# Performance work log

Measured on AMD Instinct MI355X. Metric: run time of the kernel, lower is better.

Reference implementation:

```python
import jax, jax.numpy as jnp
import numpy as np

D = 1024      # d_model
H = 16        # num_heads
HW = D // H   # head_width = 64
FF = 4 * D    # hidden_dim = 4096
BATCH = 2
T = 2048
EPS = 1e-5


def layer_norm(x, g, b):
    mu = jnp.mean(x, axis=-1, keepdims=True)
    var = jnp.mean(jnp.square(x - mu), axis=-1, keepdims=True)
    return (x - mu) * jax.lax.rsqrt(var + EPS) * g + b


def setup_inputs() -> dict:
    key = jax.random.key(0)
    ks = jax.random.split(key, 7)
    s = 0.02
    return {
        "x": jax.random.normal(ks[0], (BATCH, T, D), dtype=jnp.float32),
        "Wq": jax.random.normal(ks[1], (D, D), dtype=jnp.float32) * s,
        "Wk": jax.random.normal(ks[2], (D, D), dtype=jnp.float32) * s,
        "Wv": jax.random.normal(ks[3], (D, D), dtype=jnp.float32) * s,
        "W1": jax.random.normal(ks[4], (FF, D), dtype=jnp.float32) * s,
        "W2": jax.random.normal(ks[5], (D, FF), dtype=jnp.float32) * s,
        "g1": jnp.ones((D,), dtype=jnp.float32),
        "b1": jnp.zeros((D,), dtype=jnp.float32),
        "g2": jnp.ones((D,), dtype=jnp.float32),
        "b2": jnp.zeros((D,), dtype=jnp.float32),
    }


def reference(x, Wq, Wk, Wv, W1, W2, g1, b1, g2, b2):
    N, t, d = x.shape
    # norm1
    xn = layer_norm(x, g1, b1)

    # --- MHSA with ALiBi + causal mask (math mirrors torch module) ---
    def heads(y):  # (N,t,D) -> (N,H,t,HW)
        return y.reshape(N, t, H, HW).transpose(0, 2, 1, 3)

    q = heads(xn @ Wq.T)
    k = heads(xn @ Wk.T)
    v = heads(xn @ Wv.T)

    scores = jnp.einsum("nhqd,nhkd->nhqk", q, k) / np.sqrt(HW).astype(np.float32)

    pos = jnp.arange(t)
    rel = (pos[None, :] - pos[:, None]).astype(x.dtype)           # [t,t], rel[i,j]=j-i
    slopes = (2.0 ** (-(jnp.arange(1, H + 1)) * (8.0 / H))).astype(x.dtype)  # [H]
    alibi = slopes[:, None, None] * rel                            # [H,t,t]
    causal = jnp.where(pos[None, :] > pos[:, None],
                       jnp.array(-jnp.inf, x.dtype),
                       jnp.array(0.0, x.dtype))                    # [t,t]

    att = jax.nn.softmax(scores + alibi[None] + causal[None, None], axis=-1)
    o = jnp.einsum("nhqk,nhkd->nhqd", att, v)
    o = o.transpose(0, 2, 1, 3).reshape(N, t, d)

    att_out = xn + o

    # --- MLP: Linear -> SiLU -> Linear ---
    h = layer_norm(att_out, g2, b2)
    m = jax.nn.silu(h @ W1.T) @ W2.T
    return att_out + m
```

## Files before the change

kernel.cpp:

```cpp
#include <hip/hip_runtime.h>

#define DMODEL 1024
#define NHEAD  16
#define HWID   64
#define FFDIM  4096
#define NBATCH 2
#define SEQT   2048
#define NTOK   4096
#define QKLD   3072

using bf8    = __attribute__((ext_vector_type(8))) short;
using f32x4  = __attribute__((ext_vector_type(4))) float;
using f32x16 = __attribute__((ext_vector_type(16))) float;

__device__ inline short to_bf16(float f) {
  unsigned u = __float_as_uint(f);
  return (short)((u + 0x7fffu + ((u >> 16) & 1u)) >> 16);
}
__device__ inline float from_bf16(short s) {
  return __uint_as_float(((unsigned)(unsigned short)s) << 16);
}
__device__ inline float exp2_fast(float x) {
  float r;
  asm("v_exp_f32 %0, %1" : "=v"(r) : "v"(x));
  return r;
}
__device__ inline unsigned cvt_pk_bf16(float lo, float hi) {
  unsigned r;
  asm("v_cvt_pk_bf16_f32 %0, %1, %2" : "=v"(r) : "v"(lo), "v"(hi));
  return r;
}
__device__ inline void lds_load16(const void* g, void* l) {
  __builtin_amdgcn_global_load_lds(
      (const __attribute__((address_space(1))) void*)g,
      (__attribute__((address_space(3))) void*)l, 16, 0, 0);
}

__global__ __launch_bounds__(256)
void cvt_kernel(const float* __restrict__ in, short* __restrict__ out, int n4) {
  int i = blockIdx.x * 256 + threadIdx.x;
  if (i < n4) {
    float4 v = ((const float4*)in)[i];
    short4 o;
    o.x = to_bf16(v.x); o.y = to_bf16(v.y);
    o.z = to_bf16(v.z); o.w = to_bf16(v.w);
    ((short4*)out)[i] = o;
  }
}

__global__ __launch_bounds__(256)
void ln_kernel(const float* __restrict__ x, const float* __restrict__ g,
               const float* __restrict__ b, short* __restrict__ out) {
  const int row = blockIdx.x;
  const int t = threadIdx.x;
  const float4 v = ((const float4*)(x + (long)row * DMODEL))[t];
  float s  = v.x + v.y + v.z + v.w;
  float s2 = v.x * v.x + v.y * v.y + v.z * v.z + v.w * v.w;
#pragma unroll
  for (int m = 1; m < 64; m <<= 1) {
    s  += __shfl_xor(s, m);
    s2 += __shfl_xor(s2, m);
  }
  __shared__ float red[8];
  if ((t & 63) == 0) { red[t >> 6] = s; red[4 + (t >> 6)] = s2; }
  __syncthreads();
  s  = red[0] + red[1] + red[2] + red[3];
  s2 = red[4] + red[5] + red[6] + red[7];
  const float mu = s * (1.f / DMODEL);
  const float rs = rsqrtf(s2 * (1.f / DMODEL) - mu * mu + 1e-5f);
  const float4 gv = ((const float4*)g)[t];
  const float4 bv = ((const float4*)b)[t];
  short4 o;
  o.x = to_bf16((v.x - mu) * rs * gv.x + bv.x);
  o.y = to_bf16((v.y - mu) * rs * gv.y + bv.y);
  o.z = to_bf16((v.z - mu) * rs * gv.z + bv.z);
  o.w = to_bf16((v.w - mu) * rs * gv.w + bv.w);
  ((short4*)(out + (long)row * DMODEL))[t] = o;
}

template <int EPI>
__global__ __launch_bounds__(512)
void gemm8(const short* __restrict__ A, const short* __restrict__ Bw,
           void* __restrict__ Cout, int N, int lda, int ldb,
           int Kslice, long zstride) {
  __shared__ short lds[4][2][8192];
  const int tid = threadIdx.x;
  const int wid = tid >> 6, lane = tid & 63;
  const int wm = wid >> 2, wn = wid & 3;
  const int l15 = lane & 15, l4 = lane >> 4;

  const int gx = gridDim.x, nwg = gx * gridDim.y;
  const int wg = blockIdx.y * gx + blockIdx.x;
  const int sw = (wg & 7) * (nwg >> 3) + (wg >> 3);
  const int sx = gx >> 2;
  const int st = sw >> 4, w16 = sw & 15;
  const long bm = (long)((st / sx) * 4 + (w16 >> 2)) * 256;
  const long bn = (long)((st % sx) * 4 + (w16 & 3)) * 256;
  const int kofs = blockIdx.z * Kslice;

  long aoff[2], boff[2];
#pragma unroll
  for (int rd = 0; rd < 2; ++rd) {
    const int row = rd * 128 + (tid >> 2);
    const int slog = (tid & 3) ^ ((row >> 1) & 3);
    aoff[rd] = (bm + row) * (long)lda + slog * 8 + kofs;
    boff[rd] = (bn + row) * (long)ldb + slog * 8 + kofs;
  }
  int offA[8], offB[4];
#pragma unroll
  for (int ph = 0; ph < 2; ++ph)
#pragma unroll
    for (int m = 0; m < 4; ++m) {
      const int row = wm * 128 + ph * 64 + m * 16 + l15;
      offA[ph * 4 + m] = row * 64 + ((l4 ^ ((row >> 1) & 3)) << 4);
    }
#pragma unroll
  for (int n = 0; n < 4; ++n) {
    const int row = wn * 64 + n * 16 + l15;
    offB[n] = row * 64 + ((l4 ^ ((row >> 1) & 3)) << 4);
  }

  const int NT = Kslice >> 5;
  f32x4 acc[8][4] = {};

#pragma unroll
  for (int t = 0; t < 3; ++t) {
    char* sb = (char*)&lds[t][0][0] + wid * 1024;
    lds_load16(A  + aoff[0] + t * 32, sb);
    lds_load16(A  + aoff[1] + t * 32, sb + 8192);
    lds_load16(Bw + boff[0] + t * 32, sb + 16384);
    lds_load16(Bw + boff[1] + t * 32, sb + 24576);
  }
  asm volatile("s_waitcnt vmcnt(8)" ::: "memory");
  __builtin_amdgcn_s_barrier();
  asm volatile("" ::: "memory");

  for (int t = 0; t < NT; ++t) {
    const char* sb = (const char*)&lds[t & 3][0][0];
    char* db = (char*)&lds[(t + 3) & 3][0][0] + wid * 1024;
    const bool pf = (t + 3) < NT;
    const long ks = (long)(t + 3) * 32;
    bf8 a0[4], bb[4];
#pragma unroll
    for (int m = 0; m < 4; ++m) a0[m] = *(const bf8*)(sb + offA[m]);
#pragma unroll
    for (int n = 0; n < 4; ++n) bb[n] = *(const bf8*)(sb + 16384 + offB[n]);
    if (pf) {
      lds_load16(A + aoff[0] + ks, db);
      lds_load16(A + aoff[1] + ks, db + 8192);
    }
    __builtin_amdgcn_s_barrier();
    asm volatile("" ::: "memory");
    __builtin_amdgcn_s_setprio(1);
#pragma unroll
    for (int m = 0; m < 4; ++m)
#pragma unroll
      for (int n = 0; n < 4; ++n)
        acc[m][n] = __builtin_amdgcn_mfma_f32_16x16x32_bf16(a0[m], bb[n], acc[m][n], 0, 0, 0);
    __builtin_amdgcn_s_setprio(0);
    __builtin_amdgcn_s_barrier();
    asm volatile("" ::: "memory");
    bf8 a1[4];
#pragma unroll
    for (int m = 0; m < 4; ++m) a1[m] = *(const bf8*)(sb + offA[4 + m]);
    if (pf) {
      lds_load16(Bw + boff[0] + ks, db + 16384);
      lds_load16(Bw + boff[1] + ks, db + 24576);
    }
    const int rem = NT - 1 - t;
    if (rem >= 3)      asm volatile("s_waitcnt vmcnt(8)" ::: "memory");
    else if (rem == 2) asm volatile("s_waitcnt vmcnt(4)" ::: "memory");
    else if (rem == 1) asm volatile("s_waitcnt vmcnt(0)" ::: "memory");
    __builtin_amdgcn_s_barrier();
    asm volatile("" ::: "memory");
    __builtin_amdgcn_s_setprio(1);
#pragma unroll
    for (int m = 0; m < 4; ++m)
#pragma unroll
      for (int n = 0; n < 4; ++n)
        acc[4 + m][n] = __builtin_amdgcn_mfma_f32_16x16x32_bf16(a1[m], bb[n], acc[4 + m][n], 0, 0, 0);
    __builtin_amdgcn_s_setprio(0);
    __builtin_amdgcn_s_barrier();
    asm volatile("" ::: "memory");
  }

  float* Cp = (float*)Cout + blockIdx.z * zstride;
#pragma unroll
  for (int mg = 0; mg < 8; ++mg)
#pragma unroll
    for (int n = 0; n < 4; ++n) {
      const long col = bn + wn * 64 + n * 16 + l15;
#pragma unroll
      for (int r = 0; r < 4; ++r) {
        const long row = bm + wm * 128 + mg * 16 + l4 * 4 + r;
        float v = acc[mg][n][r];
        if (EPI == 0) {
          ((short*)Cout)[row * N + col] = to_bf16(v);
        } else if (EPI == 1) {
          ((short*)Cout)[row * N + col] = to_bf16(v / (1.f + __expf(-v)));
        } else {
          Cp[row * N + col] = v;
        }
      }
    }
}

__global__ __launch_bounds__(256)
void pack_k(const short* __restrict__ qkv, short* __restrict__ Kp) {
  const int g = blockIdx.x, bh = blockIdx.y;
  const int b = bh >> 4, h = bh & 15;
  const int t = threadIdx.x;
  const int row = t >> 3, cc = t & 7, c = cc >> 1, hi = cc & 1;
  const bf8 v = *(const bf8*)&qkv[(long)(b * SEQT + g * 32 + row) * QKLD +
                                  1024 + h * HWID + c * 16 + hi * 8];
  *(bf8*)&Kp[(((long)bh * 256 + g * 4 + c) * 64 + hi * 32 + row) * 8] = v;
}

__global__ __launch_bounds__(256)
void pack_v(const short* __restrict__ qkv, short* __restrict__ Vp) {
  __shared__ short tile[64][72];
  const int tc = blockIdx.x, bh = blockIdx.y;
  const int b = bh >> 4, h = bh & 15;
  const int t = threadIdx.x;
  {
    const int r = t >> 2, c = (t & 3) * 16;
    const long src = (long)(b * SEQT + tc * 64 + r) * QKLD + 2048 + h * HWID + c;
    *(bf8*)&tile[r][c]     = *(const bf8*)&qkv[src];
    *(bf8*)&tile[r][c + 8] = *(const bf8*)&qkv[src + 8];
  }
  __syncthreads();
  const int dg = t >> 7, ch = (t >> 5) & 3, row = t & 31;
#pragma unroll
  for (int hi = 0; hi < 2; ++hi) {
    short o[8];
#pragma unroll
    for (int j = 0; j < 8; ++j) o[j] = tile[ch * 16 + hi * 8 + j][dg * 32 + row];
    *(bf8*)&Vp[(((long)bh * 256 + dg * 128 + tc * 4 + ch) * 64 + hi * 32 + row) * 8] =
        *(bf8*)o;
  }
}

__global__ __launch_bounds__(64, 2)
void attn_kernel(const short* __restrict__ qkv, const short* __restrict__ Kp,
                 const short* __restrict__ Vp, const short* __restrict__ xn,
                 float* __restrict__ att) {
  const int L = blockIdx.x;
  const int bh = (L & 7) * 4 + ((L >> 3) & 3);
  const int qtile = 63 - (L >> 5);
  const int b = bh >> 4, h = bh & 15;
  const int q0 = qtile * 32;
  const int lane = threadIdx.x;
  const int l31 = lane & 31, hi = lane >> 5;
  const long tokbase = (long)b * SEQT;

  bf8 qf[4];
  {
    const short* qrow = qkv + (tokbase + q0 + l31) * QKLD + h * HWID + hi * 8;
#pragma unroll
    for (int c = 0; c < 4; ++c) qf[c] = *(const bf8*)(qrow + c * 16);
  }

  const float slope2 = exp2f(-0.5f * (float)(h + 1)) * 1.44269504f;
  const float sc2 = 0.125f * 1.44269504f;
  float arr[16];
#pragma unroll
  for (int r = 0; r < 16; ++r) arr[r] = slope2 * (float)((r & 3) + 8 * (r >> 2));
  const float hofs = slope2 * 4.f * (float)hi;
  const float qabs = (float)(q0 + l31);

  float m2 = -1e30f, lsum = 0.f;
  f32x16 acc0 = {}, acc1 = {};
  const int ktm = q0 >> 6;
  const bf8* kfb = (const bf8*)Kp + (long)bh * 16384 + lane;
  const bf8* vfb = (const bf8*)Vp + (long)bh * 16384 + lane;

  bf8 kc[8], kn[8], vc[8];
#pragma unroll
  for (int c = 0; c < 4; ++c) {
    kc[c]     = kfb[c * 64];
    kc[4 + c] = kfb[256 + c * 64];
  }

#pragma unroll 2
  for (int kt = 0; kt <= ktm; ++kt) {
    const int k0 = kt * 64;
    const long vb = (long)kt * 256;
#pragma unroll
    for (int ch = 0; ch < 4; ++ch) {
      vc[ch]     = vfb[vb + ch * 64];
      vc[4 + ch] = vfb[8192 + vb + ch * 64];
    }
    const long nb = (long)(kt < ktm ? kt + 1 : kt) * 512;
#pragma unroll
    for (int c = 0; c < 4; ++c) {
      kn[c]     = kfb[nb + c * 64];
      kn[4 + c] = kfb[nb + 256 + c * 64];
    }
    f32x16 s0 = {}, s1 = {};
#pragma unroll
    for (int c = 0; c < 4; ++c) {
      s0 = __builtin_amdgcn_mfma_f32_32x32x16_bf16(kc[c], qf[c], s0, 0, 0, 0);
      s1 = __builtin_amdgcn_mfma_f32_32x32x16_bf16(kc[4 + c], qf[c], s1, 0, 0, 0);
    }
    const float base = slope2 * ((float)k0 - qabs) + hofs;
    float s[32];
#pragma unroll
    for (int r = 0; r < 16; ++r) {
      s[r]      = fmaf(s0[r], sc2, base + arr[r]);
      s[16 + r] = fmaf(s1[r], sc2, base + arr[r] + slope2 * 32.f);
    }
    if (kt == ktm) {
      const int qi = q0 + l31;
#pragma unroll
      for (int r = 0; r < 16; ++r) {
        const int krel = (r & 3) + 8 * (r >> 2) + 4 * hi;
        if (k0 + krel > qi)      s[r]      = -1e30f;
        if (k0 + 32 + krel > qi) s[16 + r] = -1e30f;
      }
    }
    float ma = s[0], mb = s[1], mc = s[2], md = s[3];
#pragma unroll
    for (int i = 4; i < 32; i += 4) {
      ma = fmaxf(ma, s[i]); mb = fmaxf(mb, s[i + 1]);
      mc = fmaxf(mc, s[i + 2]); md = fmaxf(md, s[i + 3]);
    }
    float pm = fmaxf(fmaxf(ma, mb), fmaxf(mc, md));
    pm = fmaxf(pm, __shfl_xor(pm, 32));
    if (!__all(pm - m2 <= 11.0f)) {
      const float nm = fmaxf(m2, pm);
      const float alpha = exp2_fast(m2 - nm);
      m2 = nm;
      lsum *= alpha;
      acc0 *= alpha;
      acc1 *= alpha;
    }
    float p[32];
#pragma unroll
    for (int i = 0; i < 32; ++i) p[i] = exp2_fast(s[i] - m2);
    float sa = p[0], sb = p[1], sc = p[2], sd = p[3];
#pragma unroll
    for (int i = 4; i < 32; i += 4) {
      sa += p[i]; sb += p[i + 1]; sc += p[i + 2]; sd += p[i + 3];
    }
    float rs = (sa + sb) + (sc + sd);
    rs += __shfl_xor(rs, 32);
    lsum += rs;
    unsigned cpk[16];
#pragma unroll
    for (int g = 0; g < 8; ++g) {
      cpk[g]     = cvt_pk_bf16(p[2 * g], p[2 * g + 1]);
      cpk[8 + g] = cvt_pk_bf16(p[16 + 2 * g], p[16 + 2 * g + 1]);
    }
    bf8 pb[4];
#pragma unroll
    for (int ch = 0; ch < 4; ++ch) {
      const int cb = (ch >> 1) * 8 + (ch & 1) * 4;
      unsigned u0 = cpk[cb + 0], u2 = cpk[cb + 2];
      unsigned u1 = cpk[cb + 1], u3 = cpk[cb + 3];
      asm("v_permlane32_swap_b32 %0, %1" : "+v"(u0), "+v"(u2));
      asm("v_permlane32_swap_b32 %0, %1" : "+v"(u1), "+v"(u3));
      union { unsigned u[4]; bf8 v; } f;
      f.u[0] = u0; f.u[1] = u1; f.u[2] = u2; f.u[3] = u3;
      pb[ch] = f.v;
    }
#pragma unroll
    for (int ch = 0; ch < 4; ++ch) {
      acc0 = __builtin_amdgcn_mfma_f32_32x32x16_bf16(vc[ch], pb[ch], acc0, 0, 0, 0);
      acc1 = __builtin_amdgcn_mfma_f32_32x32x16_bf16(vc[4 + ch], pb[ch], acc1, 0, 0, 0);
    }
#pragma unroll
    for (int i = 0; i < 8; ++i) kc[i] = kn[i];
  }

  __shared__ float Os[32 * 68];
  const float rl = 1.f / lsum;
#pragma unroll
  for (int r = 0; r < 16; ++r) {
    const int d0 = (r & 3) + 8 * (r >> 2) + 4 * hi;
    Os[l31 * 68 + d0]      = acc0[r] * rl;
    Os[l31 * 68 + 32 + d0] = acc1[r] * rl;
  }
  __syncthreads();
#pragma unroll
  for (int it = 0; it < 8; ++it) {
    const int idx = it * 64 + lane;
    const int row = idx >> 4, c4 = idx & 15;
    const float4 ov = *(const float4*)&Os[row * 68 + c4 * 4];
    const long gbase = (tokbase + q0 + row) * DMODEL + h * HWID + c4 * 4;
    const short4 xv = *(const short4*)&xn[gbase];
    float4 o;
    o.x = ov.x + from_bf16(xv.x);
    o.y = ov.y + from_bf16(xv.y);
    o.z = ov.z + from_bf16(xv.z);
    o.w = ov.w + from_bf16(xv.w);
    *(float4*)&att[gbase] = o;
  }
}

__global__ __launch_bounds__(256)
void combine_kernel(const float* __restrict__ p, float* __restrict__ dout, int n4) {
  int i = blockIdx.x * 256 + threadIdx.x;
  if (i < n4) {
    float4 a  = ((const float4*)dout)[i];
    float4 b0 = ((const float4*)(p))[i];
    float4 b1 = ((const float4*)(p + 4194304))[i];
    float4 b2 = ((const float4*)(p + 8388608))[i];
    float4 b3 = ((const float4*)(p + 12582912))[i];
    a.x += (b0.x + b1.x) + (b2.x + b3.x);
    a.y += (b0.y + b1.y) + (b2.y + b3.y);
    a.z += (b0.z + b1.z) + (b2.z + b3.z);
    a.w += (b0.w + b1.w) + (b2.w + b3.w);
    ((float4*)dout)[i] = a;
  }
}

extern "C" void kernel_launch(void* const* d_in, const int* in_sizes, int n_in,
                              void* d_out, int out_size, void* d_ws, size_t ws_size,
                              hipStream_t stream) {
  (void)in_sizes; (void)n_in; (void)out_size; (void)ws_size;
  const float* x  = (const float*)d_in[0];
  const float* Wq = (const float*)d_in[1];
  const float* Wk = (const float*)d_in[2];
  const float* Wv = (const float*)d_in[3];
  const float* W1 = (const float*)d_in[4];
  const float* W2 = (const float*)d_in[5];
  const float* g1 = (const float*)d_in[6];
  const float* b1 = (const float*)d_in[7];
  const float* g2 = (const float*)d_in[8];
  const float* b2 = (const float*)d_in[9];

  char* ws = (char*)d_ws;
  const size_t MB = 1024 * 1024;
  short* wqkv_b = (short*)(ws + 0);
  short* w1_b   = (short*)(ws + 6  * MB);
  short* w2_b   = (short*)(ws + 14 * MB);
  short* xn     = (short*)(ws + 22 * MB);
  short* qkv    = (short*)(ws + 30 * MB);
  short* m1     = (short*)(ws + 22 * MB);
  short* Kp     = (short*)(ws + 54 * MB);
  short* Vp     = (short*)(ws + 62 * MB);
  short* hb     = (short*)(ws + 70 * MB);
  float* parts  = (float*)(ws + 54 * MB);
  float* att    = (float*)d_out;

  cvt_kernel<<<1024, 256, 0, stream>>>(Wq, wqkv_b, 262144);
  cvt_kernel<<<1024, 256, 0, stream>>>(Wk, wqkv_b + 1048576, 262144);
  cvt_kernel<<<1024, 256, 0, stream>>>(Wv, wqkv_b + 2097152, 262144);
  cvt_kernel<<<4096, 256, 0, stream>>>(W1, w1_b, 1048576);
  cvt_kernel<<<4096, 256, 0, stream>>>(W2, w2_b, 1048576);

  ln_kernel<<<NTOK, 256, 0, stream>>>(x, g1, b1, xn);

  gemm8<0><<<dim3(12, 16), 512, 0, stream>>>(xn, wqkv_b, qkv, QKLD, DMODEL, DMODEL,
                                             DMODEL, 0);
  pack_k<<<dim3(64, 32), 256, 0, stream>>>(qkv, Kp);
  pack_v<<<dim3(32, 32), 256, 0, stream>>>(qkv, Vp);

  attn_kernel<<<2048, 64, 0, stream>>>(qkv, Kp, Vp, xn, att);

  ln_kernel<<<NTOK, 256, 0, stream>>>(att, g2, b2, hb);

  gemm8<1><<<dim3(16, 16), 512, 0, stream>>>(hb, w1_b, m1, FFDIM, DMODEL, DMODEL,
                                             DMODEL, 0);
  gemm8<2><<<dim3(4, 16, 4), 512, 0, stream>>>(m1, w2_b, parts, DMODEL, FFDIM, FFDIM,
                                               1024, (long)NTOK * DMODEL);
  combine_kernel<<<4096, 256, 0, stream>>>(parts, (float*)d_out, 1048576);
}
```

Before: 216.1 us.

## Replace 256x256 GEMM with 128x128 tile, 3-stage pipeline, drop split-K

```diff
diff --git a/kernel.cpp b/kernel.cpp
--- a/kernel.cpp
+++ b/kernel.cpp
@@ -79,127 +79,108 @@
 }
 
 template <int EPI>
-__global__ __launch_bounds__(512)
-void gemm8(const short* __restrict__ A, const short* __restrict__ Bw,
-           void* __restrict__ Cout, int N, int lda, int ldb,
-           int Kslice, long zstride) {
-  __shared__ short lds[4][2][8192];
+__global__ __launch_bounds__(256, 3)
+void gemm4(const short* __restrict__ A, const short* __restrict__ Bw,
+           void* __restrict__ Cout, int N, int lda, int ldb, int K) {
+  __shared__ short lds[3][2][4096];
   const int tid = threadIdx.x;
-  const int wid = tid >> 6, lane = tid & 63;
-  const int wm = wid >> 2, wn = wid & 3;
+  const int w = tid >> 6, lane = tid & 63;
   const int l15 = lane & 15, l4 = lane >> 4;
+  const int wr = (w >> 1) * 64, wc = (w & 1) * 64;
 
   const int gx = gridDim.x, nwg = gx * gridDim.y;
   const int wg = blockIdx.y * gx + blockIdx.x;
   const int sw = (wg & 7) * (nwg >> 3) + (wg >> 3);
   const int sx = gx >> 2;
   const int st = sw >> 4, w16 = sw & 15;
-  const long bm = (long)((st / sx) * 4 + (w16 >> 2)) * 256;
-  const long bn = (long)((st % sx) * 4 + (w16 & 3)) * 256;
-  const int kofs = blockIdx.z * Kslice;
+  const long bm = (long)((st / sx) * 4 + (w16 >> 2)) * 128;
+  const long bn = (long)((st % sx) * 4 + (w16 & 3)) * 128;
 
   long aoff[2], boff[2];
 #pragma unroll
-  for (int rd = 0; rd < 2; ++rd) {
-    const int row = rd * 128 + (tid >> 2);
-    const int slog = (tid & 3) ^ ((row >> 1) & 3);
-    aoff[rd] = (bm + row) * (long)lda + slog * 8 + kofs;
-    boff[rd] = (bn + row) * (long)ldb + slog * 8 + kofs;
-  }
-  int offA[8], offB[4];
-#pragma unroll
-  for (int ph = 0; ph < 2; ++ph)
-#pragma unroll
-    for (int m = 0; m < 4; ++m) {
-      const int row = wm * 128 + ph * 64 + m * 16 + l15;
-      offA[ph * 4 + m] = row * 64 + ((l4 ^ ((row >> 1) & 3)) << 4);
-    }
+  for (int i = 0; i < 2; ++i) {
+    const int c = i * 4 + w;
+    const int row = c * 16 + (lane >> 2);
+    const int slog = (lane & 3) ^ ((row >> 1) & 3);
+    aoff[i] = (bm + row) * (long)lda + slog * 8;
+    boff[i] = (bn + row) * (long)ldb + slog * 8;
+  }
+  int offA[4], offB[4];
+#pragma unroll
+  for (int m = 0; m < 4; ++m) {
+    const int row = wr + m * 16 + l15;
+    offA[m] = row * 64 + ((l4 ^ ((row >> 1) & 3)) << 4);
+  }
 #pragma unroll
   for (int n = 0; n < 4; ++n) {
-    const int row = wn * 64 + n * 16 + l15;
+    const int row = wc + n * 16 + l15;
     offB[n] = row * 64 + ((l4 ^ ((row >> 1) & 3)) << 4);
   }
 
-  const int NT = Kslice >> 5;
-  f32x4 acc[8][4] = {};
-
-#pragma unroll
-  for (int t = 0; t < 3; ++t) {
-    char* sb = (char*)&lds[t][0][0] + wid * 1024;
-    lds_load16(A  + aoff[0] + t * 32, sb);
-    lds_load16(A  + aoff[1] + t * 32, sb + 8192);
-    lds_load16(Bw + boff[0] + t * 32, sb + 16384);
-    lds_load16(Bw + boff[1] + t * 32, sb + 24576);
-  }
-  asm volatile("s_waitcnt vmcnt(8)" ::: "memory");
-  __builtin_amdgcn_s_barrier();
-  asm volatile("" ::: "memory");
-
+  const int NT = K >> 5;
+  f32x4 acc[4][4] = {};
+
+#pragma unroll
+  for (int t = 0; t < 2; ++t) {
+    char* db = (char*)&lds[t][0][0];
+#pragma unroll
+    for (int i = 0; i < 2; ++i) {
+      const int c = i * 4 + w;
+      lds_load16(A  + aoff[i] + t * 32, db + c * 1024);
+      lds_load16(Bw + boff[i] + t * 32, db + 8192 + c * 1024);
+    }
+  }
+
+  int slot = 0, pslot = 2;
   for (int t = 0; t < NT; ++t) {
-    const char* sb = (const char*)&lds[t & 3][0][0];
-    char* db = (char*)&lds[(t + 3) & 3][0][0] + wid * 1024;
-    const bool pf = (t + 3) < NT;
-    const long ks = (long)(t + 3) * 32;
-    bf8 a0[4], bb[4];
-#pragma unroll
-    for (int m = 0; m < 4; ++m) a0[m] = *(const bf8*)(sb + offA[m]);
-#pragma unroll
-    for (int n = 0; n < 4; ++n) bb[n] = *(const bf8*)(sb + 16384 + offB[n]);
-    if (pf) {
-      lds_load16(A + aoff[0] + ks, db);
-      lds_load16(A + aoff[1] + ks, db + 8192);
-    }
+    if (t + 1 < NT) asm volatile("s_waitcnt vmcnt(4)" ::: "memory");
+    else            asm volatile("s_waitcnt vmcnt(0)" ::: "memory");
     __builtin_amdgcn_s_barrier();
     asm volatile("" ::: "memory");
+    if (t + 2 < NT) {
+      char* db = (char*)&lds[pslot][0][0];
+      const long ks = (long)(t + 2) * 32;
+#pragma unroll
+      for (int i = 0; i < 2; ++i) {
+        const int c = i * 4 + w;
+        lds_load16(A  + aoff[i] + ks, db + c * 1024);
+        lds_load16(Bw + boff[i] + ks, db + 8192 + c * 1024);
+      }
+    }
+    const char* sb = (const char*)&lds[slot][0][0];
+    bf8 af[4], bfr[4];
+#pragma unroll
+    for (int m = 0; m < 4; ++m) af[m] = *(const bf8*)(sb + offA[m]);
+#pragma unroll
+    for (int n = 0; n < 4; ++n) bfr[n] = *(const bf8*)(sb + 8192 + offB[n]);
     __builtin_amdgcn_s_setprio(1);
 #pragma unroll
     for (int m = 0; m < 4; ++m)
 #pragma unroll
       for (int n = 0; n < 4; ++n)
-        acc[m][n] = __builtin_amdgcn_mfma_f32_16x16x32_bf16(a0[m], bb[n], acc[m][n], 0, 0, 0);
+        acc[m][n] = __builtin_amdgcn_mfma_f32_16x16x32_bf16(af[m], bfr[n], acc[m][n], 0, 0, 0);
     __builtin_amdgcn_s_setprio(0);
-    __builtin_amdgcn_s_barrier();
-    asm volatile("" ::: "memory");
-    bf8 a1[4];
-#pragma unroll
-    for (int m = 0; m < 4; ++m) a1[m] = *(const bf8*)(sb + offA[4 + m]);
-    if (pf) {
-      lds_load16(Bw + boff[0] + ks, db + 16384);
-      lds_load16(Bw + boff[1] + ks, db + 24576);
-    }
-    const int rem = NT - 1 - t;
-    if (rem >= 3)      asm volatile("s_waitcnt vmcnt(8)" ::: "memory");
-    else if (rem == 2) asm volatile("s_waitcnt vmcnt(4)" ::: "memory");
-    else if (rem == 1) asm volatile("s_waitcnt vmcnt(0)" ::: "memory");
-    __builtin_amdgcn_s_barrier();
-    asm volatile("" ::: "memory");
-    __builtin_amdgcn_s_setprio(1);
-#pragma unroll
-    for (int m = 0; m < 4; ++m)
-#pragma unroll
-      for (int n = 0; n < 4; ++n)
-        acc[4 + m][n] = __builtin_amdgcn_mfma_f32_16x16x32_bf16(a1[m], bb[n], acc[4 + m][n], 0, 0, 0);
-    __builtin_amdgcn_s_setprio(0);
-    __builtin_amdgcn_s_barrier();
-    asm volatile("" ::: "memory");
-  }
-
-  float* Cp = (float*)Cout + blockIdx.z * zstride;
-#pragma unroll
-  for (int mg = 0; mg < 8; ++mg)
+    slot  = (slot  == 2) ? 0 : slot  + 1;
+    pslot = (pslot == 2) ? 0 : pslot + 1;
+  }
+
+#pragma unroll
+  for (int m = 0; m < 4; ++m)
 #pragma unroll
     for (int n = 0; n < 4; ++n) {
-      const long col = bn + wn * 64 + n * 16 + l15;
+      const long col = bn + wc + n * 16 + l15;
 #pragma unroll
       for (int r = 0; r < 4; ++r) {
-        const long row = bm + wm * 128 + mg * 16 + l4 * 4 + r;
-        float v = acc[mg][n][r];
+        const long row = bm + wr + m * 16 + l4 * 4 + r;
+        float v = acc[m][n][r];
         if (EPI == 0) {
           ((short*)Cout)[row * N + col] = to_bf16(v);
         } else if (EPI == 1) {
           ((short*)Cout)[row * N + col] = to_bf16(v / (1.f + __expf(-v)));
         } else {
-          Cp[row * N + col] = v;
+          float* Cp = (float*)Cout;
+          const long idx = row * N + col;
+          Cp[idx] = Cp[idx] + v;
         }
       }
     }
@@ -394,23 +375,6 @@
     o.z = ov.z + from_bf16(xv.z);
     o.w = ov.w + from_bf16(xv.w);
     *(float4*)&att[gbase] = o;
-  }
-}
-
-__global__ __launch_bounds__(256)
-void combine_kernel(const float* __restrict__ p, float* __restrict__ dout, int n4) {
-  int i = blockIdx.x * 256 + threadIdx.x;
-  if (i < n4) {
-    float4 a  = ((const float4*)dout)[i];
-    float4 b0 = ((const float4*)(p))[i];
-    float4 b1 = ((const float4*)(p + 4194304))[i];
-    float4 b2 = ((const float4*)(p + 8388608))[i];
-    float4 b3 = ((const float4*)(p + 12582912))[i];
-    a.x += (b0.x + b1.x) + (b2.x + b3.x);
-    a.y += (b0.y + b1.y) + (b2.y + b3.y);
-    a.z += (b0.z + b1.z) + (b2.z + b3.z);
-    a.w += (b0.w + b1.w) + (b2.w + b3.w);
-    ((float4*)dout)[i] = a;
   }
 }
 
@@ -440,7 +404,6 @@
   short* Kp     = (short*)(ws + 54 * MB);
   short* Vp     = (short*)(ws + 62 * MB);
   short* hb     = (short*)(ws + 70 * MB);
-  float* parts  = (float*)(ws + 54 * MB);
   float* att    = (float*)d_out;
 
   cvt_kernel<<<1024, 256, 0, stream>>>(Wq, wqkv_b, 262144);
@@ -451,8 +414,7 @@
 
   ln_kernel<<<NTOK, 256, 0, stream>>>(x, g1, b1, xn);
 
-  gemm8<0><<<dim3(12, 16), 512, 0, stream>>>(xn, wqkv_b, qkv, QKLD, DMODEL, DMODEL,
-                                             DMODEL, 0);
+  gemm4<0><<<dim3(24, 32), 256, 0, stream>>>(xn, wqkv_b, qkv, QKLD, DMODEL, DMODEL, DMODEL);
   pack_k<<<dim3(64, 32), 256, 0, stream>>>(qkv, Kp);
   pack_v<<<dim3(32, 32), 256, 0, stream>>>(qkv, Vp);
 
@@ -460,9 +422,6 @@
 
   ln_kernel<<<NTOK, 256, 0, stream>>>(att, g2, b2, hb);
 
-  gemm8<1><<<dim3(16, 16), 512, 0, stream>>>(hb, w1_b, m1, FFDIM, DMODEL, DMODEL,
-                                             DMODEL, 0);
-  gemm8<2><<<dim3(4, 16, 4), 512, 0, stream>>>(m1, w2_b, parts, DMODEL, FFDIM, FFDIM,
-                                               1024, (long)NTOK * DMODEL);
-  combine_kernel<<<4096, 256, 0, stream>>>(parts, (float*)d_out, 1048576);
-}
+  gemm4<1><<<dim3(32, 32), 256, 0, stream>>>(hb, w1_b, m1, FFDIM, DMODEL, DMODEL, DMODEL);
+  gemm4<2><<<dim3(8, 32), 256, 0, stream>>>(m1, w2_b, d_out, DMODEL, FFDIM, FFDIM, FFDIM);
+}
```

Result: no change. 218.9 us (+1.3%).
